# Optimization experiments

Hardware: AMD Instinct MI355X
Metric: run time of the kernel (lower is better)

## Reference

```python
import jax, jax.numpy as jnp
import numpy as np
import math

C = 768; H = 12; B = 2; TX = 2048; TC = 2048

def setup_inputs() -> dict:
    key = jax.random.key(0)
    ks = jax.random.split(key, 20)
    w = lambda k, s: jax.random.normal(k, s, dtype=jnp.float32) * 0.02
    inp = {
        "x": jax.random.normal(ks[0], (B, TX, C), dtype=jnp.float32),
        "context": jax.random.normal(ks[1], (B, TC, C), dtype=jnp.float32),
        "ln1_g": jnp.ones((C,), jnp.float32), "ln1_b": jnp.zeros((C,), jnp.float32),
        "ln2_g": jnp.ones((C,), jnp.float32), "ln2_b": jnp.zeros((C,), jnp.float32),
        "ln3_g": jnp.ones((C,), jnp.float32), "ln3_b": jnp.zeros((C,), jnp.float32),
        "sa_wq": w(ks[2], (C, C)), "sa_bq": jnp.zeros((C,), jnp.float32),
        "sa_wk": w(ks[3], (C, C)), "sa_bk": jnp.zeros((C,), jnp.float32),
        "sa_wv": w(ks[4], (C, C)), "sa_bv": jnp.zeros((C,), jnp.float32),
        "sa_wo": w(ks[5], (C, C)), "sa_bo": jnp.zeros((C,), jnp.float32),
        "xa_wq": w(ks[6], (C, C)), "xa_bq": jnp.zeros((C,), jnp.float32),
        "xa_wk": w(ks[7], (C, C)), "xa_bk": jnp.zeros((C,), jnp.float32),
        "xa_wv": w(ks[8], (C, C)), "xa_bv": jnp.zeros((C,), jnp.float32),
        "xa_wo": w(ks[9], (C, C)), "xa_bo": jnp.zeros((C,), jnp.float32),
        "mlp_w1": w(ks[10], (C, 4 * C)), "mlp_b1": jnp.zeros((4 * C,), jnp.float32),
        "mlp_w2": w(ks[11], (4 * C, C)), "mlp_b2": jnp.zeros((C,), jnp.float32),
        "n_head": H,
    }
    return inp

def _layernorm(x, g, b, eps=1e-5):
    mu = jnp.mean(x, axis=-1, keepdims=True)
    var = jnp.mean(jnp.square(x - mu), axis=-1, keepdims=True)
    return (x - mu) * jax.lax.rsqrt(var + eps) * g + b

def _attn(xq, xkv, wq, bq, wk, bk, wv, bv, wo, bo, n_head):
    Bq, Tq, Cm = xq.shape
    Tk = xkv.shape[1]
    dh = Cm // n_head
    q = (xq @ wq + bq).reshape(Bq, Tq, n_head, dh)
    k = (xkv @ wk + bk).reshape(Bq, Tk, n_head, dh)
    v = (xkv @ wv + bv).reshape(Bq, Tk, n_head, dh)
    att = jnp.einsum('bqhd,bkhd->bhqk', q, k) * (1.0 / math.sqrt(dh))
    att = jax.nn.softmax(att, axis=-1)
    y = jnp.einsum('bhqk,bkhd->bqhd', att, v).reshape(Bq, Tq, Cm)
    return y @ wo + bo

def reference(x, context, ln1_g, ln1_b, ln2_g, ln2_b, ln3_g, ln3_b,
              sa_wq, sa_bq, sa_wk, sa_bk, sa_wv, sa_bv, sa_wo, sa_bo,
              xa_wq, xa_bq, xa_wk, xa_bk, xa_wv, xa_bv, xa_wo, xa_bo,
              mlp_w1, mlp_b1, mlp_w2, mlp_b2, n_head):
    # pre-LN residual self-attention
    x = x + _attn(_layernorm(x, ln1_g, ln1_b), _layernorm(x, ln1_g, ln1_b),
                  sa_wq, sa_bq, sa_wk, sa_bk, sa_wv, sa_bv, sa_wo, sa_bo, n_head)
    # pre-LN residual cross-attention (context not normalized, matching source)
    x = x + _attn(_layernorm(x, ln2_g, ln2_b), context,
                  xa_wq, xa_bq, xa_wk, xa_bk, xa_wv, xa_bv, xa_wo, xa_bo, n_head)
    # pre-LN residual MLP with exact (erf) GELU, as torch.nn.GELU default
    h = _layernorm(x, ln3_g, ln3_b)
    x = x + (jax.nn.gelu(h @ mlp_w1 + mlp_b1, approximate=False) @ mlp_w2 + mlp_b2)
    return (x, context)
```

## Files before the change

kernel.cpp:

```cpp
#include <hip/hip_runtime.h>
#include <hip/hip_bf16.h>
#include <math.h>

#define CDIM 768
#define HDIM 3072
#define NROWS 4096
#define TSEQ 2048
#define NHEAD 12
#define KVSPLIT 4
#define KVLEN (TSEQ / KVSPLIT)

typedef unsigned short u16;
typedef unsigned int   u32;
typedef __attribute__((ext_vector_type(8))) short short8;
typedef __attribute__((ext_vector_type(4))) float f32x4;

#define QSCALE 0.18033688011112042f

static __device__ __forceinline__ u16 f2bf(float f) {
    u32 x = __float_as_uint(f);
    x += 0x7fffu + ((x >> 16) & 1u);
    return (u16)(x >> 16);
}
static __device__ __forceinline__ float bf2f(u16 x) {
    return __uint_as_float((u32)x << 16);
}
static __device__ __forceinline__ u32 cvt_pk_bf16(float lo, float hi) {
    u32 r;
    asm("v_cvt_pk_bf16_f32 %0, %1, %2" : "=v"(r) : "v"(lo), "v"(hi));
    return r;
}

#define GLL16(g, l)                                                            \
    __builtin_amdgcn_global_load_lds(                                          \
        (const __attribute__((address_space(1))) void*)(g),                    \
        (__attribute__((address_space(3))) void*)(l), 16, 0, 0)

__launch_bounds__(256)
__global__ void wtrans(const float* __restrict__ w, u16* __restrict__ wt,
                       int K, int N) {
    __shared__ float t[32][33];
    const int n0 = blockIdx.x * 32, k0 = blockIdx.y * 32;
    const int tx = threadIdx.x & 31, ty = threadIdx.x >> 5;
#pragma unroll
    for (int i = ty; i < 32; i += 8)
        t[i][tx] = w[(size_t)(k0 + i) * N + n0 + tx];
    __syncthreads();
#pragma unroll
    for (int i = ty; i < 32; i += 8)
        wt[(size_t)(n0 + i) * K + k0 + tx] = f2bf(t[tx][i]);
}

struct WT3 { const float* w[3]; u16* wt[3]; };
__launch_bounds__(256)
__global__ void wtrans3(WT3 a) {
    __shared__ float t[32][33];
    const float* __restrict__ w = a.w[blockIdx.z];
    u16* __restrict__ wt = a.wt[blockIdx.z];
    const int n0 = blockIdx.x * 32, k0 = blockIdx.y * 32;
    const int tx = threadIdx.x & 31, ty = threadIdx.x >> 5;
#pragma unroll
    for (int i = ty; i < 32; i += 8)
        t[i][tx] = w[(size_t)(k0 + i) * CDIM + n0 + tx];
    __syncthreads();
#pragma unroll
    for (int i = ty; i < 32; i += 8)
        wt[(size_t)(n0 + i) * CDIM + k0 + tx] = f2bf(t[tx][i]);
}

__launch_bounds__(256)
__global__ void cvt_copy(const float* __restrict__ in, u16* __restrict__ out,
                         int n4) {
    int i = blockIdx.x * 256 + threadIdx.x;
    if (i >= n4) return;
    float4 v = ((const float4*)in)[i];
    ushort4 o;
    o.x = f2bf(v.x); o.y = f2bf(v.y); o.z = f2bf(v.z); o.w = f2bf(v.w);
    ((ushort4*)out)[i] = o;
}

__launch_bounds__(256)
__global__ void ln_kernel(const float* __restrict__ x, const float* __restrict__ g,
                          const float* __restrict__ bta, u16* __restrict__ out) {
    const int row = blockIdx.x, tid = threadIdx.x;
    const float* xr = x + (size_t)row * CDIM;
    float v0 = xr[tid], v1 = xr[tid + 256], v2 = xr[tid + 512];
    __shared__ float red[8];
    float s = v0 + v1 + v2;
#pragma unroll
    for (int m = 1; m < 64; m <<= 1) s += __shfl_xor(s, m);
    if ((tid & 63) == 0) red[tid >> 6] = s;
    __syncthreads();
    const float mu = (red[0] + red[1] + red[2] + red[3]) * (1.f / CDIM);
    const float d0 = v0 - mu, d1 = v1 - mu, d2 = v2 - mu;
    float q = d0 * d0 + d1 * d1 + d2 * d2;
#pragma unroll
    for (int m = 1; m < 64; m <<= 1) q += __shfl_xor(q, m);
    if ((tid & 63) == 0) red[4 + (tid >> 6)] = q;
    __syncthreads();
    const float var = (red[4] + red[5] + red[6] + red[7]) * (1.f / CDIM);
    const float rstd = rsqrtf(var + 1e-5f);
    u16* orow = out + (size_t)row * CDIM;
    orow[tid]       = f2bf(d0 * rstd * g[tid]       + bta[tid]);
    orow[tid + 256] = f2bf(d1 * rstd * g[tid + 256] + bta[tid + 256]);
    orow[tid + 512] = f2bf(d2 * rstd * g[tid + 512] + bta[tid + 512]);
}

struct GemmArgs {
    const u16* A[3];
    const u16* BT[3];
    const float* bias[3];
    const float* res[3];
    void* out[3];
    float alpha[3];
    int M, N, K;
};

template <int EPI, int BM, int BN = 128>
__launch_bounds__(256)
__global__ void gemm_bt(GemmArgs ga) {
    constexpr int MF = BM / 32, NF = BN / 32;
    __shared__ u16 Abuf[BM * 32];
    __shared__ u16 Bbuf[BN * 32];
    const int z = blockIdx.z;
    const u16* __restrict__ A  = ga.A[z];
    const u16* __restrict__ BT = ga.BT[z];
    const float* __restrict__ bias = ga.bias[z];
    const float* __restrict__ res  = ga.res[z];
    void* outv = ga.out[z];
    const float alpha = ga.alpha[z];
    const int N = ga.N, K = ga.K;

    const int tid = threadIdx.x;
    const int lane = tid & 63, w = tid >> 6;
    const int m0 = blockIdx.x * BM, n0 = blockIdx.y * BN;
    const int wr = (w >> 1) * (BM / 2), wc = (w & 1) * (BN / 2);
    const int lr = lane & 15, lc = lane >> 4;

    const int srowA = (BM == 128) ? (w * 32 + (lane >> 2)) : (tid >> 2);
    const int srowB = (BN == 128) ? (w * 32 + (lane >> 2)) : (tid >> 2);
    const int scol = (lane & 3) * 8;
    const u16* Ag = A + (size_t)(m0 + srowA) * K + scol;
    const u16* Bg = BT + (size_t)(n0 + srowB) * K + scol;
    char* Ab = (char*)Abuf + w * (BM == 128 ? 2048 : 1024);
    char* Bb = (char*)Bbuf + w * (BN == 128 ? 2048 : 1024);

    f32x4 acc[MF][NF];
#pragma unroll
    for (int m = 0; m < MF; ++m)
#pragma unroll
        for (int n = 0; n < NF; ++n) acc[m][n] = (f32x4){0.f, 0.f, 0.f, 0.f};

    const int nk = K >> 5;
    for (int kt = 0; kt < nk; ++kt) {
        const int ko = kt * 32;
        GLL16(Ag + ko, Ab);
        if constexpr (BM == 128) GLL16(Ag + 16 * K + ko, Ab + 1024);
        GLL16(Bg + ko, Bb);
        if constexpr (BN == 128) GLL16(Bg + 16 * K + ko, Bb + 1024);
        __syncthreads();
        short8 af[MF], bfv[NF];
#pragma unroll
        for (int m = 0; m < MF; ++m)
            af[m] = *(const short8*)((const char*)Abuf +
                                     (size_t)(wr + m * 16 + lr) * 64 + lc * 16);
#pragma unroll
        for (int n = 0; n < NF; ++n)
            bfv[n] = *(const short8*)((const char*)Bbuf +
                                      (size_t)(wc + n * 16 + lr) * 64 + lc * 16);
#pragma unroll
        for (int m = 0; m < MF; ++m)
#pragma unroll
            for (int n = 0; n < NF; ++n)
                acc[m][n] = __builtin_amdgcn_mfma_f32_16x16x32_bf16(
                    af[m], bfv[n], acc[m][n], 0, 0, 0);
        __syncthreads();
    }

#pragma unroll
    for (int n = 0; n < NF; ++n) {
        const int gc = n0 + wc + n * 16 + lr;
        const float bs = bias[gc];
#pragma unroll
        for (int m = 0; m < MF; ++m) {
            const int gr = m0 + wr + m * 16 + lc * 4;
#pragma unroll
            for (int r = 0; r < 4; ++r) {
                float v = (acc[m][n][r] + bs) * alpha;
                const size_t idx = (size_t)(gr + r) * N + gc;
                if constexpr (EPI == 0) {
                    ((u16*)outv)[idx] = f2bf(v);
                } else if constexpr (EPI == 1) {
                    ((float*)outv)[idx] = res[idx] + v;
                } else {
                    float gel = 0.5f * v * (1.0f + erff(v * 0.70710678118654752f));
                    ((u16*)outv)[idx] = f2bf(gel);
                }
            }
        }
    }
}

__launch_bounds__(256)
__global__ void attn_split(const u16* __restrict__ Qb, const u16* __restrict__ Kb,
                           const u16* __restrict__ Vb, u16* __restrict__ Opart,
                           float2* __restrict__ ml) {
    __shared__ u16 Klds[64 * 72];
    __shared__ u16 Vt[64 * 72];
    const int tid = threadIdx.x;
    const int lane = tid & 63, w = tid >> 6;
    const int lr = lane & 15, lc = lane >> 4;
    const int b = blockIdx.y / NHEAD, h = blockIdx.y % NHEAD;
    const int z = blockIdx.z;
    const size_t qrow0 = (size_t)b * TSEQ + blockIdx.x * 64 + w * 16;
    const size_t krow0 = (size_t)b * TSEQ + (size_t)z * KVLEN;
    const int hc = h * 64;

    short8 qf0, qf1;
    {
        const u16* qp = Qb + (qrow0 + lr) * CDIM + hc + lc * 8;
        qf0 = *(const short8*)qp;
        qf1 = *(const short8*)(qp + 32);
    }
    f32x4 oacc[4];
#pragma unroll
    for (int r = 0; r < 4; ++r) oacc[r] = (f32x4){0.f, 0.f, 0.f, 0.f};
    float mrow = -3e38f, lrow = 0.f;

    const int stg_r = tid >> 2, stg_s = tid & 3;
    const u16* kg = Kb + (krow0 + stg_r) * CDIM + hc + stg_s * 16;
    const u16* vg = Vb + (krow0 + stg_r) * CDIM + hc + stg_s * 16;
    uint4 ka0 = *(const uint4*)kg, ka1 = *(const uint4*)(kg + 8);
    uint4 va0 = *(const uint4*)vg, va1 = *(const uint4*)(vg + 8);
    const int sig = ((stg_r >> 5) << 5) + (((stg_r >> 2) & 3) << 3) +
                    (((stg_r >> 4) & 1) << 2) + (stg_r & 3);
    char* vdst = (char*)Vt + ((2 * sig) ^ (stg_s << 5)) +
                 (size_t)(stg_s * 16) * 144;

    for (int kt = 0; kt < KVLEN / 64; ++kt) {
        __syncthreads();
        {
            *(uint4*)&Klds[stg_r * 72 + stg_s * 16]     = ka0;
            *(uint4*)&Klds[stg_r * 72 + stg_s * 16 + 8] = ka1;
            u16 tmp[16];
            *(uint4*)(tmp)     = va0;
            *(uint4*)(tmp + 8) = va1;
#pragma unroll
            for (int j = 0; j < 16; ++j)
                *(u16*)(vdst + (size_t)j * 144) = tmp[j];
        }
        if (kt < KVLEN / 64 - 1) {
            kg += 64 * CDIM; vg += 64 * CDIM;
            ka0 = *(const uint4*)kg; ka1 = *(const uint4*)(kg + 8);
            va0 = *(const uint4*)vg; va1 = *(const uint4*)(vg + 8);
        }
        __syncthreads();

        f32x4 sf[4];
#pragma unroll
        for (int fn = 0; fn < 4; ++fn) {
            const u16* kr = &Klds[(lr + fn * 16) * 72 + lc * 8];
            short8 kb0 = *(const short8*)kr;
            short8 kb1 = *(const short8*)(kr + 32);
            f32x4 t = (f32x4){0.f, 0.f, 0.f, 0.f};
            t = __builtin_amdgcn_mfma_f32_16x16x32_bf16(kb0, qf0, t, 0, 0, 0);
            t = __builtin_amdgcn_mfma_f32_16x16x32_bf16(kb1, qf1, t, 0, 0, 0);
            sf[fn] = t;
        }

        float pm;
        {
            float a0 = fmaxf(fmaxf(sf[0][0], sf[0][1]), fmaxf(sf[0][2], sf[0][3]));
            float a1 = fmaxf(fmaxf(sf[1][0], sf[1][1]), fmaxf(sf[1][2], sf[1][3]));
            float a2 = fmaxf(fmaxf(sf[2][0], sf[2][1]), fmaxf(sf[2][2], sf[2][3]));
            float a3 = fmaxf(fmaxf(sf[3][0], sf[3][1]), fmaxf(sf[3][2], sf[3][3]));
            pm = fmaxf(fmaxf(a0, a1), fmaxf(a2, a3));
            pm = fmaxf(pm, __shfl_xor(pm, 16));
            pm = fmaxf(pm, __shfl_xor(pm, 32));
        }
        if (!__all(pm <= mrow)) {
            const float mn = fmaxf(mrow, pm);
            const float corr = exp2f(mrow - mn);
            mrow = mn;
            lrow *= corr;
#pragma unroll
            for (int fd = 0; fd < 4; ++fd)
#pragma unroll
                for (int r = 0; r < 4; ++r) oacc[fd][r] *= corr;
        }
        float rs;
        {
#pragma unroll
            for (int fn = 0; fn < 4; ++fn)
#pragma unroll
                for (int r = 0; r < 4; ++r) sf[fn][r] = exp2f(sf[fn][r] - mrow);
            float s0 = (sf[0][0] + sf[0][1]) + (sf[0][2] + sf[0][3]);
            float s1 = (sf[1][0] + sf[1][1]) + (sf[1][2] + sf[1][3]);
            float s2 = (sf[2][0] + sf[2][1]) + (sf[2][2] + sf[2][3]);
            float s3 = (sf[3][0] + sf[3][1]) + (sf[3][2] + sf[3][3]);
            rs = (s0 + s1) + (s2 + s3);
            rs += __shfl_xor(rs, 16);
            rs += __shfl_xor(rs, 32);
        }
        lrow += rs;

        int4 pw0, pw1;
        pw0.x = cvt_pk_bf16(sf[0][0], sf[0][1]);
        pw0.y = cvt_pk_bf16(sf[0][2], sf[0][3]);
        pw0.z = cvt_pk_bf16(sf[1][0], sf[1][1]);
        pw0.w = cvt_pk_bf16(sf[1][2], sf[1][3]);
        pw1.x = cvt_pk_bf16(sf[2][0], sf[2][1]);
        pw1.y = cvt_pk_bf16(sf[2][2], sf[2][3]);
        pw1.z = cvt_pk_bf16(sf[3][0], sf[3][1]);
        pw1.w = cvt_pk_bf16(sf[3][2], sf[3][3]);
        short8 pb0 = *(short8*)&pw0;
        short8 pb1 = *(short8*)&pw1;

#pragma unroll
        for (int fd = 0; fd < 4; ++fd) {
            const char* vtb = (const char*)Vt + (size_t)(lr + fd * 16) * 144;
            short8 vb0 = *(const short8*)(vtb + ((lc * 16) ^ (fd * 32)));
            short8 vb1 = *(const short8*)(vtb + ((lc * 16 + 64) ^ (fd * 32)));
            oacc[fd] = __builtin_amdgcn_mfma_f32_16x16x32_bf16(vb0, pb0, oacc[fd], 0, 0, 0);
            oacc[fd] = __builtin_amdgcn_mfma_f32_16x16x32_bf16(vb1, pb1, oacc[fd], 0, 0, 0);
        }
    }

    u16* obase = Opart + (size_t)z * NROWS * CDIM + (qrow0 + lr) * CDIM + hc + lc * 4;
#pragma unroll
    for (int fd = 0; fd < 4; ++fd) {
        ushort4 o;
        o.x = f2bf(oacc[fd][0]); o.y = f2bf(oacc[fd][1]);
        o.z = f2bf(oacc[fd][2]); o.w = f2bf(oacc[fd][3]);
        *(ushort4*)(obase + fd * 16) = o;
    }
    if (lc == 0)
        ml[((size_t)z * NROWS + qrow0 + lr) * NHEAD + h] = (float2){mrow, lrow};
}

__launch_bounds__(256)
__global__ void attn_merge4(const u16* __restrict__ P, const float2* __restrict__ ml,
                            u16* __restrict__ out) {
    const int i4 = blockIdx.x * 256 + threadIdx.x;
    const size_t base = (size_t)i4 * 4;
    const int row = (int)(base / CDIM);
    const int head = (int)(base - (size_t)row * CDIM) >> 6;
    float2 a[KVSPLIT];
    float M = -3e38f;
#pragma unroll
    for (int z = 0; z < KVSPLIT; ++z) {
        a[z] = ml[((size_t)z * NROWS + row) * NHEAD + head];
        M = fmaxf(M, a[z].x);
    }
    float den = 0.f, e[KVSPLIT];
#pragma unroll
    for (int z = 0; z < KVSPLIT; ++z) {
        e[z] = exp2f(a[z].x - M);
        den += a[z].y * e[z];
    }
    const float rden = 1.f / den;
    float o0 = 0.f, o1 = 0.f, o2 = 0.f, o3 = 0.f;
#pragma unroll
    for (int z = 0; z < KVSPLIT; ++z) {
        ushort4 p = *(const ushort4*)(P + (size_t)z * NROWS * CDIM + base);
        o0 += bf2f(p.x) * e[z];
        o1 += bf2f(p.y) * e[z];
        o2 += bf2f(p.z) * e[z];
        o3 += bf2f(p.w) * e[z];
    }
    ushort4 o;
    o.x = f2bf(o0 * rden); o.y = f2bf(o1 * rden);
    o.z = f2bf(o2 * rden); o.w = f2bf(o3 * rden);
    *(ushort4*)(out + base) = o;
}

extern "C" void kernel_launch(void* const* d_in, const int* in_sizes, int n_in,
                              void* d_out, int out_size, void* d_ws, size_t ws_size,
                              hipStream_t stream) {
    const float* x     = (const float*)d_in[0];
    const float* ctx   = (const float*)d_in[1];
    const float* ln1g  = (const float*)d_in[2];
    const float* ln1b  = (const float*)d_in[3];
    const float* ln2g  = (const float*)d_in[4];
    const float* ln2b  = (const float*)d_in[5];
    const float* ln3g  = (const float*)d_in[6];
    const float* ln3b  = (const float*)d_in[7];
    const float* sa_wq = (const float*)d_in[8];
    const float* sa_bq = (const float*)d_in[9];
    const float* sa_wk = (const float*)d_in[10];
    const float* sa_bk = (const float*)d_in[11];
    const float* sa_wv = (const float*)d_in[12];
    const float* sa_bv = (const float*)d_in[13];
    const float* sa_wo = (const float*)d_in[14];
    const float* sa_bo = (const float*)d_in[15];
    const float* xa_wq = (const float*)d_in[16];
    const float* xa_bq = (const float*)d_in[17];
    const float* xa_wk = (const float*)d_in[18];
    const float* xa_bk = (const float*)d_in[19];
    const float* xa_wv = (const float*)d_in[20];
    const float* xa_bv = (const float*)d_in[21];
    const float* xa_wo = (const float*)d_in[22];
    const float* xa_bo = (const float*)d_in[23];
    const float* m_w1  = (const float*)d_in[24];
    const float* m_b1  = (const float*)d_in[25];
    const float* m_w2  = (const float*)d_in[26];
    const float* m_b2  = (const float*)d_in[27];

    float* out_x   = (float*)d_out;
    float* out_ctx = out_x + (size_t)NROWS * CDIM;
    u16* Opart = (u16*)d_out;

    const size_t SZ_ACT  = (size_t)NROWS * CDIM * 2;
    const size_t SZ_WBIG = (size_t)HDIM * CDIM * 2;
    const size_t SZ_R    = (size_t)NROWS * CDIM * 4;
    const size_t NEEDED  = 5 * SZ_ACT + SZ_R + SZ_WBIG;
    if (ws_size < NEEDED) return;

    char* ws = (char*)d_ws;
    u16* qb    = (u16*)(ws);
    u16* kb    = (u16*)(ws + 1 * SZ_ACT);
    u16* vb    = (u16*)(ws + 2 * SZ_ACT);
    u16* ctxb  = (u16*)(ws + 3 * SZ_ACT);
    u16* hb    = qb;
    u16* lnbuf = (u16*)(ws + 4 * SZ_ACT);
    u16* attB  = lnbuf;
    float* R   = (float*)(ws + 5 * SZ_ACT);
    u16* Wq    = (u16*)(ws + 5 * SZ_ACT + SZ_R);
    u16* Wk    = Wq + (size_t)CDIM * CDIM;
    u16* Wv    = Wk + (size_t)CDIM * CDIM;
    float2* ml = (float2*)Wq;

    const dim3 tb(256);
    GemmArgs ga;
    WT3 wg;

    cvt_copy<<<dim3(3072), tb, 0, stream>>>(ctx, ctxb, NROWS * CDIM / 4);

    ln_kernel<<<dim3(NROWS), tb, 0, stream>>>(x, ln1g, ln1b, lnbuf);
    wg.w[0] = sa_wq; wg.w[1] = sa_wk; wg.w[2] = sa_wv;
    wg.wt[0] = Wq;   wg.wt[1] = Wk;   wg.wt[2] = Wv;
    wtrans3<<<dim3(24, 24, 3), tb, 0, stream>>>(wg);
    ga = GemmArgs{};
    ga.A[0] = lnbuf; ga.BT[0] = Wq; ga.bias[0] = sa_bq; ga.out[0] = qb; ga.alpha[0] = QSCALE;
    ga.A[1] = lnbuf; ga.BT[1] = Wk; ga.bias[1] = sa_bk; ga.out[1] = kb; ga.alpha[1] = 1.f;
    ga.A[2] = lnbuf; ga.BT[2] = Wv; ga.bias[2] = sa_bv; ga.out[2] = vb; ga.alpha[2] = 1.f;
    ga.M = 4096; ga.N = 768; ga.K = 768;
    gemm_bt<0, 128><<<dim3(32, 6, 3), tb, 0, stream>>>(ga);
    attn_split<<<dim3(32, 24, KVSPLIT), tb, 0, stream>>>(qb, kb, vb, Opart, ml);
    attn_merge4<<<dim3(NROWS * CDIM / 1024), tb, 0, stream>>>(Opart, ml, attB);
    wtrans<<<dim3(24, 24), tb, 0, stream>>>(sa_wo, Wq, 768, 768);
    ga = GemmArgs{};
    ga.A[0] = attB; ga.BT[0] = Wq; ga.bias[0] = sa_bo; ga.res[0] = x; ga.out[0] = R; ga.alpha[0] = 1.f;
    ga.M = 4096; ga.N = 768; ga.K = 768;
    gemm_bt<1, 64, 64><<<dim3(64, 12, 1), tb, 0, stream>>>(ga);

    ln_kernel<<<dim3(NROWS), tb, 0, stream>>>(R, ln2g, ln2b, lnbuf);
    wg.w[0] = xa_wq; wg.w[1] = xa_wk; wg.w[2] = xa_wv;
    wg.wt[0] = Wq;   wg.wt[1] = Wk;   wg.wt[2] = Wv;
    wtrans3<<<dim3(24, 24, 3), tb, 0, stream>>>(wg);
    ga = GemmArgs{};
    ga.A[0] = lnbuf; ga.BT[0] = Wq; ga.bias[0] = xa_bq; ga.out[0] = qb; ga.alpha[0] = QSCALE;
    ga.A[1] = ctxb;  ga.BT[1] = Wk; ga.bias[1] = xa_bk; ga.out[1] = kb; ga.alpha[1] = 1.f;
    ga.A[2] = ctxb;  ga.BT[2] = Wv; ga.bias[2] = xa_bv; ga.out[2] = vb; ga.alpha[2] = 1.f;
    ga.M = 4096; ga.N = 768; ga.K = 768;
    gemm_bt<0, 128><<<dim3(32, 6, 3), tb, 0, stream>>>(ga);
    attn_split<<<dim3(32, 24, KVSPLIT), tb, 0, stream>>>(qb, kb, vb, Opart, ml);
    attn_merge4<<<dim3(NROWS * CDIM / 1024), tb, 0, stream>>>(Opart, ml, attB);
    hipMemcpyAsync(out_ctx, ctx, (size_t)NROWS * CDIM * 4,
                   hipMemcpyDeviceToDevice, stream);
    wtrans<<<dim3(24, 24), tb, 0, stream>>>(xa_wo, Wq, 768, 768);
    ga = GemmArgs{};
    ga.A[0] = attB; ga.BT[0] = Wq; ga.bias[0] = xa_bo; ga.res[0] = R; ga.out[0] = R; ga.alpha[0] = 1.f;
    ga.M = 4096; ga.N = 768; ga.K = 768;
    gemm_bt<1, 64, 64><<<dim3(64, 12, 1), tb, 0, stream>>>(ga);

    ln_kernel<<<dim3(NROWS), tb, 0, stream>>>(R, ln3g, ln3b, lnbuf);
    wtrans<<<dim3(96, 24), tb, 0, stream>>>(m_w1, Wq, 768, 3072);
    ga = GemmArgs{};
    ga.A[0] = lnbuf; ga.BT[0] = Wq; ga.bias[0] = m_b1; ga.out[0] = hb; ga.alpha[0] = 1.f;
    ga.M = 4096; ga.N = 3072; ga.K = 768;
    gemm_bt<2, 128><<<dim3(32, 24, 1), tb, 0, stream>>>(ga);
    wtrans<<<dim3(24, 96), tb, 0, stream>>>(m_w2, Wq, 3072, 768);
    ga = GemmArgs{};
    ga.A[0] = hb; ga.BT[0] = Wq; ga.bias[0] = m_b2; ga.res[0] = R; ga.out[0] = out_x; ga.alpha[0] = 1.f;
    ga.M = 4096; ga.N = 768; ga.K = 3072;
    gemm_bt<1, 64, 64><<<dim3(64, 12, 1), tb, 0, stream>>>(ga);

    (void)in_sizes; (void)n_in; (void)out_size;
}
```

Measured before the change: 362.4 us.

## Process two query tiles per attention wave and fold Wo transpose into QKV transpose

The split-KV attention kernel now has each wave handle two 16-row query tiles, so a block covers 128 query rows and each K/V tile staged in LDS is reused for twice as many queries. The grid along the query dimension is halved to match. The per-tile online-softmax step is factored into a helper that is called once per query tile. Separately, the output-projection weight transpose is folded into the batched QKV transpose launch (now four matrices), writing to its own workspace slot and removing one launch per attention block. The cost is higher register pressure from doubled accumulators, which `__launch_bounds__(256,4)` constrains, and fewer blocks in the attention grid.

```diff
diff --git a/kernel.cpp b/kernel.cpp
--- a/kernel.cpp
+++ b/kernel.cpp
@@ -51,9 +51,9 @@
         wt[(size_t)(n0 + i) * K + k0 + tx] = f2bf(t[tx][i]);
 }
 
-struct WT3 { const float* w[3]; u16* wt[3]; };
+struct WT4 { const float* w[4]; u16* wt[4]; };
 __launch_bounds__(256)
-__global__ void wtrans3(WT3 a) {
+__global__ void wtrans4(WT4 a) {
     __shared__ float t[32][33];
     const float* __restrict__ w = a.w[blockIdx.z];
     u16* __restrict__ wt = a.wt[blockIdx.z];
@@ -201,7 +201,58 @@
     }
 }
 
-__launch_bounds__(256)
+static __device__ __forceinline__ void softmax_pack(f32x4 sf[4], float& mrow,
+                                                    float& lrow, f32x4 oacc[4],
+                                                    short8& p0, short8& p1) {
+    float pm;
+    {
+        float a0 = fmaxf(fmaxf(sf[0][0], sf[0][1]), fmaxf(sf[0][2], sf[0][3]));
+        float a1 = fmaxf(fmaxf(sf[1][0], sf[1][1]), fmaxf(sf[1][2], sf[1][3]));
+        float a2 = fmaxf(fmaxf(sf[2][0], sf[2][1]), fmaxf(sf[2][2], sf[2][3]));
+        float a3 = fmaxf(fmaxf(sf[3][0], sf[3][1]), fmaxf(sf[3][2], sf[3][3]));
+        pm = fmaxf(fmaxf(a0, a1), fmaxf(a2, a3));
+        pm = fmaxf(pm, __shfl_xor(pm, 16));
+        pm = fmaxf(pm, __shfl_xor(pm, 32));
+    }
+    if (!__all(pm <= mrow)) {
+        const float mn = fmaxf(mrow, pm);
+        const float corr = exp2f(mrow - mn);
+        mrow = mn;
+        lrow *= corr;
+#pragma unroll
+        for (int fd = 0; fd < 4; ++fd)
+#pragma unroll
+            for (int r = 0; r < 4; ++r) oacc[fd][r] *= corr;
+    }
+#pragma unroll
+    for (int fn = 0; fn < 4; ++fn)
+#pragma unroll
+        for (int r = 0; r < 4; ++r) sf[fn][r] = exp2f(sf[fn][r] - mrow);
+    float rs;
+    {
+        float s0 = (sf[0][0] + sf[0][1]) + (sf[0][2] + sf[0][3]);
+        float s1 = (sf[1][0] + sf[1][1]) + (sf[1][2] + sf[1][3]);
+        float s2 = (sf[2][0] + sf[2][1]) + (sf[2][2] + sf[2][3]);
+        float s3 = (sf[3][0] + sf[3][1]) + (sf[3][2] + sf[3][3]);
+        rs = (s0 + s1) + (s2 + s3);
+        rs += __shfl_xor(rs, 16);
+        rs += __shfl_xor(rs, 32);
+    }
+    lrow += rs;
+    int4 pw0, pw1;
+    pw0.x = cvt_pk_bf16(sf[0][0], sf[0][1]);
+    pw0.y = cvt_pk_bf16(sf[0][2], sf[0][3]);
+    pw0.z = cvt_pk_bf16(sf[1][0], sf[1][1]);
+    pw0.w = cvt_pk_bf16(sf[1][2], sf[1][3]);
+    pw1.x = cvt_pk_bf16(sf[2][0], sf[2][1]);
+    pw1.y = cvt_pk_bf16(sf[2][2], sf[2][3]);
+    pw1.z = cvt_pk_bf16(sf[3][0], sf[3][1]);
+    pw1.w = cvt_pk_bf16(sf[3][2], sf[3][3]);
+    p0 = *(short8*)&pw0;
+    p1 = *(short8*)&pw1;
+}
+
+__launch_bounds__(256, 4)
 __global__ void attn_split(const u16* __restrict__ Qb, const u16* __restrict__ Kb,
                            const u16* __restrict__ Vb, u16* __restrict__ Opart,
                            float2* __restrict__ ml) {
@@ -212,20 +263,27 @@
     const int lr = lane & 15, lc = lane >> 4;
     const int b = blockIdx.y / NHEAD, h = blockIdx.y % NHEAD;
     const int z = blockIdx.z;
-    const size_t qrow0 = (size_t)b * TSEQ + blockIdx.x * 64 + w * 16;
+    const size_t qrowA = (size_t)b * TSEQ + blockIdx.x * 128 + w * 16;
+    const size_t qrowB = qrowA + 64;
     const size_t krow0 = (size_t)b * TSEQ + (size_t)z * KVLEN;
     const int hc = h * 64;
 
-    short8 qf0, qf1;
+    short8 qa0, qa1, qb0, qb1;
     {
-        const u16* qp = Qb + (qrow0 + lr) * CDIM + hc + lc * 8;
-        qf0 = *(const short8*)qp;
-        qf1 = *(const short8*)(qp + 32);
-    }
-    f32x4 oacc[4];
-#pragma unroll
-    for (int r = 0; r < 4; ++r) oacc[r] = (f32x4){0.f, 0.f, 0.f, 0.f};
-    float mrow = -3e38f, lrow = 0.f;
+        const u16* qp = Qb + (qrowA + lr) * CDIM + hc + lc * 8;
+        qa0 = *(const short8*)qp;
+        qa1 = *(const short8*)(qp + 32);
+        const u16* qp2 = Qb + (qrowB + lr) * CDIM + hc + lc * 8;
+        qb0 = *(const short8*)qp2;
+        qb1 = *(const short8*)(qp2 + 32);
+    }
+    f32x4 oaccA[4], oaccB[4];
+#pragma unroll
+    for (int r = 0; r < 4; ++r) {
+        oaccA[r] = (f32x4){0.f, 0.f, 0.f, 0.f};
+        oaccB[r] = (f32x4){0.f, 0.f, 0.f, 0.f};
+    }
+    float mA = -3e38f, lA = 0.f, mB = -3e38f, lB = 0.f;
 
     const int stg_r = tid >> 2, stg_s = tid & 3;
     const u16* kg = Kb + (krow0 + stg_r) * CDIM + hc + stg_s * 16;
@@ -256,86 +314,54 @@
         }
         __syncthreads();
 
-        f32x4 sf[4];
+        f32x4 sfA[4], sfB[4];
 #pragma unroll
         for (int fn = 0; fn < 4; ++fn) {
             const u16* kr = &Klds[(lr + fn * 16) * 72 + lc * 8];
             short8 kb0 = *(const short8*)kr;
             short8 kb1 = *(const short8*)(kr + 32);
             f32x4 t = (f32x4){0.f, 0.f, 0.f, 0.f};
-            t = __builtin_amdgcn_mfma_f32_16x16x32_bf16(kb0, qf0, t, 0, 0, 0);
-            t = __builtin_amdgcn_mfma_f32_16x16x32_bf16(kb1, qf1, t, 0, 0, 0);
-            sf[fn] = t;
+            t = __builtin_amdgcn_mfma_f32_16x16x32_bf16(kb0, qa0, t, 0, 0, 0);
+            t = __builtin_amdgcn_mfma_f32_16x16x32_bf16(kb1, qa1, t, 0, 0, 0);
+            sfA[fn] = t;
+            f32x4 u = (f32x4){0.f, 0.f, 0.f, 0.f};
+            u = __builtin_amdgcn_mfma_f32_16x16x32_bf16(kb0, qb0, u, 0, 0, 0);
+            u = __builtin_amdgcn_mfma_f32_16x16x32_bf16(kb1, qb1, u, 0, 0, 0);
+            sfB[fn] = u;
         }
 
-        float pm;
-        {
-            float a0 = fmaxf(fmaxf(sf[0][0], sf[0][1]), fmaxf(sf[0][2], sf[0][3]));
-            float a1 = fmaxf(fmaxf(sf[1][0], sf[1][1]), fmaxf(sf[1][2], sf[1][3]));
-            float a2 = fmaxf(fmaxf(sf[2][0], sf[2][1]), fmaxf(sf[2][2], sf[2][3]));
-            float a3 = fmaxf(fmaxf(sf[3][0], sf[3][1]), fmaxf(sf[3][2], sf[3][3]));
-            pm = fmaxf(fmaxf(a0, a1), fmaxf(a2, a3));
-            pm = fmaxf(pm, __shfl_xor(pm, 16));
-            pm = fmaxf(pm, __shfl_xor(pm, 32));
-        }
-        if (!__all(pm <= mrow)) {
-            const float mn = fmaxf(mrow, pm);
-            const float corr = exp2f(mrow - mn);
-            mrow = mn;
-            lrow *= corr;
-#pragma unroll
-            for (int fd = 0; fd < 4; ++fd)
-#pragma unroll
-                for (int r = 0; r < 4; ++r) oacc[fd][r] *= corr;
-        }
-        float rs;
-        {
-#pragma unroll
-            for (int fn = 0; fn < 4; ++fn)
-#pragma unroll
-                for (int r = 0; r < 4; ++r) sf[fn][r] = exp2f(sf[fn][r] - mrow);
-            float s0 = (sf[0][0] + sf[0][1]) + (sf[0][2] + sf[0][3]);
-            float s1 = (sf[1][0] + sf[1][1]) + (sf[1][2] + sf[1][3]);
-            float s2 = (sf[2][0] + sf[2][1]) + (sf[2][2] + sf[2][3]);
-            float s3 = (sf[3][0] + sf[3][1]) + (sf[3][2] + sf[3][3]);
-            rs = (s0 + s1) + (s2 + s3);
-            rs += __shfl_xor(rs, 16);
-            rs += __shfl_xor(rs, 32);
-        }
-        lrow += rs;
-
-        int4 pw0, pw1;
-        pw0.x = cvt_pk_bf16(sf[0][0], sf[0][1]);
-        pw0.y = cvt_pk_bf16(sf[0][2], sf[0][3]);
-        pw0.z = cvt_pk_bf16(sf[1][0], sf[1][1]);
-        pw0.w = cvt_pk_bf16(sf[1][2], sf[1][3]);
-        pw1.x = cvt_pk_bf16(sf[2][0], sf[2][1]);
-        pw1.y = cvt_pk_bf16(sf[2][2], sf[2][3]);
-        pw1.z = cvt_pk_bf16(sf[3][0], sf[3][1]);
-        pw1.w = cvt_pk_bf16(sf[3][2], sf[3][3]);
-        short8 pb0 = *(short8*)&pw0;
-        short8 pb1 = *(short8*)&pw1;
+        short8 pA0, pA1, pB0, pB1;
+        softmax_pack(sfA, mA, lA, oaccA, pA0, pA1);
+        softmax_pack(sfB, mB, lB, oaccB, pB0, pB1);
 
 #pragma unroll
         for (int fd = 0; fd < 4; ++fd) {
             const char* vtb = (const char*)Vt + (size_t)(lr + fd * 16) * 144;
             short8 vb0 = *(const short8*)(vtb + ((lc * 16) ^ (fd * 32)));
             short8 vb1 = *(const short8*)(vtb + ((lc * 16 + 64) ^ (fd * 32)));
-            oacc[fd] = __builtin_amdgcn_mfma_f32_16x16x32_bf16(vb0, pb0, oacc[fd], 0, 0, 0);
-            oacc[fd] = __builtin_amdgcn_mfma_f32_16x16x32_bf16(vb1, pb1, oacc[fd], 0, 0, 0);
+            oaccA[fd] = __builtin_amdgcn_mfma_f32_16x16x32_bf16(vb0, pA0, oaccA[fd], 0, 0, 0);
+            oaccA[fd] = __builtin_amdgcn_mfma_f32_16x16x32_bf16(vb1, pA1, oaccA[fd], 0, 0, 0);
+            oaccB[fd] = __builtin_amdgcn_mfma_f32_16x16x32_bf16(vb0, pB0, oaccB[fd], 0, 0, 0);
+            oaccB[fd] = __builtin_amdgcn_mfma_f32_16x16x32_bf16(vb1, pB1, oaccB[fd], 0, 0, 0);
         }
     }
 
-    u16* obase = Opart + (size_t)z * NROWS * CDIM + (qrow0 + lr) * CDIM + hc + lc * 4;
+    u16* oA = Opart + (size_t)z * NROWS * CDIM + (qrowA + lr) * CDIM + hc + lc * 4;
+    u16* oB = Opart + (size_t)z * NROWS * CDIM + (qrowB + lr) * CDIM + hc + lc * 4;
 #pragma unroll
     for (int fd = 0; fd < 4; ++fd) {
         ushort4 o;
-        o.x = f2bf(oacc[fd][0]); o.y = f2bf(oacc[fd][1]);
-        o.z = f2bf(oacc[fd][2]); o.w = f2bf(oacc[fd][3]);
-        *(ushort4*)(obase + fd * 16) = o;
-    }
-    if (lc == 0)
-        ml[((size_t)z * NROWS + qrow0 + lr) * NHEAD + h] = (float2){mrow, lrow};
+        o.x = f2bf(oaccA[fd][0]); o.y = f2bf(oaccA[fd][1]);
+        o.z = f2bf(oaccA[fd][2]); o.w = f2bf(oaccA[fd][3]);
+        *(ushort4*)(oA + fd * 16) = o;
+        o.x = f2bf(oaccB[fd][0]); o.y = f2bf(oaccB[fd][1]);
+        o.z = f2bf(oaccB[fd][2]); o.w = f2bf(oaccB[fd][3]);
+        *(ushort4*)(oB + fd * 16) = o;
+    }
+    if (lc == 0) {
+        ml[((size_t)z * NROWS + qrowA + lr) * NHEAD + h] = (float2){mA, lA};
+        ml[((size_t)z * NROWS + qrowB + lr) * NHEAD + h] = (float2){mB, lB};
+    }
 }
 
 __launch_bounds__(256)
@@ -428,49 +454,48 @@
     u16* Wq    = (u16*)(ws + 5 * SZ_ACT + SZ_R);
     u16* Wk    = Wq + (size_t)CDIM * CDIM;
     u16* Wv    = Wk + (size_t)CDIM * CDIM;
+    u16* Wo    = Wv + (size_t)CDIM * CDIM;
     float2* ml = (float2*)Wq;
 
     const dim3 tb(256);
     GemmArgs ga;
-    WT3 wg;
+    WT4 wg;
 
     cvt_copy<<<dim3(3072), tb, 0, stream>>>(ctx, ctxb, NROWS * CDIM / 4);
 
     ln_kernel<<<dim3(NROWS), tb, 0, stream>>>(x, ln1g, ln1b, lnbuf);
-    wg.w[0] = sa_wq; wg.w[1] = sa_wk; wg.w[2] = sa_wv;
-    wg.wt[0] = Wq;   wg.wt[1] = Wk;   wg.wt[2] = Wv;
-    wtrans3<<<dim3(24, 24, 3), tb, 0, stream>>>(wg);
+    wg.w[0] = sa_wq; wg.w[1] = sa_wk; wg.w[2] = sa_wv; wg.w[3] = sa_wo;
+    wg.wt[0] = Wq;   wg.wt[1] = Wk;   wg.wt[2] = Wv;   wg.wt[3] = Wo;
+    wtrans4<<<dim3(24, 24, 4), tb, 0, stream>>>(wg);
     ga = GemmArgs{};
     ga.A[0] = lnbuf; ga.BT[0] = Wq; ga.bias[0] = sa_bq; ga.out[0] = qb; ga.alpha[0] = QSCALE;
     ga.A[1] = lnbuf; ga.BT[1] = Wk; ga.bias[1] = sa_bk; ga.out[1] = kb; ga.alpha[1] = 1.f;
     ga.A[2] = lnbuf; ga.BT[2] = Wv; ga.bias[2] = sa_bv; ga.out[2] = vb; ga.alpha[2] = 1.f;
     ga.M = 4096; ga.N = 768; ga.K = 768;
     gemm_bt<0, 128><<<dim3(32, 6, 3), tb, 0, stream>>>(ga);
-    attn_split<<<dim3(32, 24, KVSPLIT), tb, 0, stream>>>(qb, kb, vb, Opart, ml);
+    attn_split<<<dim3(16, 24, KVSPLIT), tb, 0, stream>>>(qb, kb, vb, Opart, ml);
     attn_merge4<<<dim3(NROWS * CDIM / 1024), tb, 0, stream>>>(Opart, ml, attB);
-    wtrans<<<dim3(24, 24), tb, 0, stream>>>(sa_wo, Wq, 768, 768);
     ga = GemmArgs{};
-    ga.A[0] = attB; ga.BT[0] = Wq; ga.bias[0] = sa_bo; ga.res[0] = x; ga.out[0] = R; ga.alpha[0] = 1.f;
+    ga.A[0] = attB; ga.BT[0] = Wo; ga.bias[0] = sa_bo; ga.res[0] = x; ga.out[0] = R; ga.alpha[0] = 1.f;
     ga.M = 4096; ga.N = 768; ga.K = 768;
     gemm_bt<1, 64, 64><<<dim3(64, 12, 1), tb, 0, stream>>>(ga);
 
     ln_kernel<<<dim3(NROWS), tb, 0, stream>>>(R, ln2g, ln2b, lnbuf);
-    wg.w[0] = xa_wq; wg.w[1] = xa_wk; wg.w[2] = xa_wv;
-    wg.wt[0] = Wq;   wg.wt[1] = Wk;   wg.wt[2] = Wv;
-    wtrans3<<<dim3(24, 24, 3), tb, 0, stream>>>(wg);
+    wg.w[0] = xa_wq; wg.w[1] = xa_wk; wg.w[2] = xa_wv; wg.w[3] = xa_wo;
+    wg.wt[0] = Wq;   wg.wt[1] = Wk;   wg.wt[2] = Wv;   wg.wt[3] = Wo;
+    wtrans4<<<dim3(24, 24, 4), tb, 0, stream>>>(wg);
     ga = GemmArgs{};
     ga.A[0] = lnbuf; ga.BT[0] = Wq; ga.bias[0] = xa_bq; ga.out[0] = qb; ga.alpha[0] = QSCALE;
     ga.A[1] = ctxb;  ga.BT[1] = Wk; ga.bias[1] = xa_bk; ga.out[1] = kb; ga.alpha[1] = 1.f;
     ga.A[2] = ctxb;  ga.BT[2] = Wv; ga.bias[2] = xa_bv; ga.out[2] = vb; ga.alpha[2] = 1.f;
     ga.M = 4096; ga.N = 768; ga.K = 768;
     gemm_bt<0, 128><<<dim3(32, 6, 3), tb, 0, stream>>>(ga);
-    attn_split<<<dim3(32, 24, KVSPLIT), tb, 0, stream>>>(qb, kb, vb, Opart, ml);
+    attn_split<<<dim3(16, 24, KVSPLIT), tb, 0, stream>>>(qb, kb, vb, Opart, ml);
     attn_merge4<<<dim3(NROWS * CDIM / 1024), tb, 0, stream>>>(Opart, ml, attB);
     hipMemcpyAsync(out_ctx, ctx, (size_t)NROWS * CDIM * 4,
                    hipMemcpyDeviceToDevice, stream);
-    wtrans<<<dim3(24, 24), tb, 0, stream>>>(xa_wo, Wq, 768, 768);
     ga = GemmArgs{};
-    ga.A[0] = attB; ga.BT[0] = Wq; ga.bias[0] = xa_bo; ga.res[0] = R; ga.out[0] = R; ga.alpha[0] = 1.f;
+    ga.A[0] = attB; ga.BT[0] = Wo; ga.bias[0] = xa_bo; ga.res[0] = R; ga.out[0] = R; ga.alpha[0] = 1.f;
     ga.M = 4096; ga.N = 768; ga.K = 768;
     gemm_bt<1, 64, 64><<<dim3(64, 12, 1), tb, 0, stream>>>(ga);
 
```

Result: faster. 340.7 us (-6.0%).
